# Optimization experiments

Hardware: AMD Instinct MI355X
Metric: run time of the kernel (lower is better)

The kernel has to match this reference:

```python
import jax, jax.numpy as jnp
import numpy as np

B, P, M = 16, 16384, 2048
D_Z, D_PHI, D_R = 512, 256, 64
H1, H2 = 96, 96
IN_DIM = D_Z + 3 * D_PHI + D_R  # 1344


def setup_inputs() -> dict:
    key = jax.random.key(0)
    ks = jax.random.split(key, 8)
    g_q = jax.random.normal(ks[0], (B, D_Z), dtype=jnp.float32)
    Phi = jax.random.normal(ks[1], (M, D_PHI), dtype=jnp.float32)
    # pair indices with i < j (sort each row)
    pi = jax.random.randint(ks[2], (P, 2), 0, M, dtype=jnp.int64)
    pair_index = jnp.sort(pi, axis=-1)
    relation_features = jax.random.normal(ks[3], (P, D_R), dtype=jnp.float32)
    # learned MLP params (Linear weights stored [in, out])
    W1 = jax.random.normal(ks[4], (IN_DIM, H1), dtype=jnp.float32) / np.sqrt(IN_DIM)
    b1 = jnp.zeros((H1,), dtype=jnp.float32)
    W2 = jax.random.normal(ks[5], (H1, H2), dtype=jnp.float32) / np.sqrt(H1)
    b2 = jnp.zeros((H2,), dtype=jnp.float32)
    W3 = jax.random.normal(ks[6], (H2, 1), dtype=jnp.float32) / np.sqrt(H2)
    b3 = jnp.zeros((1,), dtype=jnp.float32)
    return {"g_q": g_q, "Phi": Phi, "pair_index": pair_index,
            "relation_features": relation_features,
            "W1": W1, "b1": b1, "W2": W2, "b2": b2, "W3": W3, "b3": b3}


def reference(g_q, Phi, pair_index, relation_features, W1, b1, W2, b2, W3, b3):
    # gather pair embeddings: [P, d_phi]
    phi_i = Phi[pair_index[:, 0]]
    phi_j = Phi[pair_index[:, 1]]
    # symmetric combine -> [P, 3*d_phi + d_r]
    pair_feats = jnp.concatenate(
        [phi_i + phi_j, jnp.abs(phi_i - phi_j), phi_i * phi_j, relation_features],
        axis=-1)
    b, p = g_q.shape[0], pair_feats.shape[0]
    # broadcast-concat -> x: [B, P, in_dim]
    x = jnp.concatenate(
        [jnp.broadcast_to(g_q[:, None, :], (b, p, g_q.shape[-1])),
         jnp.broadcast_to(pair_feats[None, :, :], (b, p, pair_feats.shape[-1]))],
        axis=-1)
    # small MLP: Linear -> GELU (erf, dropout is identity at eval) x2, then Linear(->1)
    h = jax.nn.gelu(x @ W1 + b1, approximate=False)
    h = jax.nn.gelu(h @ W2 + b2, approximate=False)
    out = h @ W3 + b3  # [B, P, 1]
    return out[..., 0]  # [B, P]
```

## Files before the change

kernel.cpp:

```cpp
#include <hip/hip_runtime.h>
#include <hip/hip_bf16.h>
#include <stdint.h>

static constexpr int P_N   = 16384;
static constexpr int D_Z   = 512;
static constexpr int D_PHI = 256;
static constexpr int D_R   = 64;
static constexpr int H     = 96;
static constexpr int KP    = 832;

using f32x4 = __attribute__((ext_vector_type(4))) float;
using s16x8 = __attribute__((ext_vector_type(8))) short;

__device__ __forceinline__ unsigned short f2bf(float f) {
    union { float f; uint32_t u; } v; v.f = f;
    return (unsigned short)((v.u + 0x7FFFu + ((v.u >> 16) & 1u)) >> 16);
}

__device__ __forceinline__ uint32_t pkbf2(float lo, float hi) {
    union { __hip_bfloat162 h; uint32_t u; } c;
    c.h = __float22bfloat162_rn(make_float2(lo, hi));
    return c.u;
}

__device__ __forceinline__ float gelu_f(float x) {
    float x2 = x * x;
    float u  = __builtin_fmaf(-0.1029444f, x2, -2.3022126f);
    float e  = __builtin_amdgcn_exp2f(x * u);
    return x * __builtin_amdgcn_rcpf(1.0f + e);
}

__global__ __launch_bounds__(256) void prep_kernel(
    const float* __restrict__ g_q, const float* __restrict__ W1,
    const float* __restrict__ b1, const float* __restrict__ W2,
    float* __restrict__ gqfrag, unsigned short* __restrict__ W1frag,
    unsigned short* __restrict__ W2frag)
{
    __shared__ float gql[D_Z];
    __shared__ float red[192];
    const int blk = blockIdx.x;
    const int t = threadIdx.x;
    if (blk < 16) {
        const int b = blk;
        for (int i = t; i < D_Z; i += 256) gql[i] = g_q[b * D_Z + i];
        __syncthreads();
        float acc = 0.f;
        if (t < 192) {
            const int n = t % 96, s = t / 96;
            const int k0 = s * 256;
            #pragma unroll 8
            for (int k = 0; k < 256; ++k)
                acc += gql[k0 + k] * W1[(k0 + k) * H + n];
            red[t] = acc;
        }
        __syncthreads();
        if (t < 96) {
            const float v = red[t] + red[t + 96] + b1[t];
            const int dst = ((t >> 5) * 64 + ((t >> 3) & 3) * 16 + b) * 8 + (t & 7);
            gqfrag[dst] = v;
        }
    } else if (blk < 328) {
        const int e = (blk - 16) * 256 + t;
        const int n = e / KP, k = e % KP;
        const int nf = n >> 4, lr = n & 15;
        const int kc = k >> 5, l4 = (k >> 3) & 3, ke = k & 7;
        W1frag[((nf * 26 + kc) * 64 + l4 * 16 + lr) * 8 + ke] =
            f2bf(W1[(D_Z + k) * H + n]);
    } else {
        const int e = (blk - 328) * 256 + t;
        const int n = e / H, k = e % H;
        const int nf = n >> 4, lr = n & 15;
        const int ks = k >> 5, l4 = (k >> 3) & 3, ke = k & 7;
        W2frag[((nf * 3 + ks) * 64 + l4 * 16 + lr) * 8 + ke] =
            f2bf(W2[k * H + n]);
    }
}

__global__ __launch_bounds__(512, 2) void fused11_kernel(
    const float* __restrict__ Phi, const int* __restrict__ pidx,
    const float* __restrict__ rel, const unsigned short* __restrict__ W1frag,
    const float* __restrict__ gqfrag, const unsigned short* __restrict__ W2frag,
    const float* __restrict__ b2, const float* __restrict__ W3,
    const float* __restrict__ b3, float* __restrict__ out)
{
    constexpr int FS = 840;
    __shared__ __align__(16) unsigned short feats[16 * FS];
    __shared__ __align__(16) float y1part[2][16][100];
    const int t = threadIdx.x;
    const int p0 = blockIdx.x * 16;

    {
        const int p = t >> 5, c = t & 31, kb = c * 8;
        const int2 ij = *(const int2*)(pidx + 2 * (p0 + p));
        const float* PI = Phi + (long)ij.x * D_PHI + kb;
        const float* PJ = Phi + (long)ij.y * D_PHI + kb;
        float4 a0 = *(const float4*)PI, a1 = *(const float4*)(PI + 4);
        float4 c0 = *(const float4*)PJ, c1 = *(const float4*)(PJ + 4);
        uint4 s, d, q;
        s.x = pkbf2(a0.x + c0.x, a0.y + c0.y);
        s.y = pkbf2(a0.z + c0.z, a0.w + c0.w);
        s.z = pkbf2(a1.x + c1.x, a1.y + c1.y);
        s.w = pkbf2(a1.z + c1.z, a1.w + c1.w);
        d.x = pkbf2(fabsf(a0.x - c0.x), fabsf(a0.y - c0.y));
        d.y = pkbf2(fabsf(a0.z - c0.z), fabsf(a0.w - c0.w));
        d.z = pkbf2(fabsf(a1.x - c1.x), fabsf(a1.y - c1.y));
        d.w = pkbf2(fabsf(a1.z - c1.z), fabsf(a1.w - c1.w));
        q.x = pkbf2(a0.x * c0.x, a0.y * c0.y);
        q.y = pkbf2(a0.z * c0.z, a0.w * c0.w);
        q.z = pkbf2(a1.x * c1.x, a1.y * c1.y);
        q.w = pkbf2(a1.z * c1.z, a1.w * c1.w);
        *(uint4*)&feats[p * FS + kb]       = s;
        *(uint4*)&feats[p * FS + 256 + kb] = d;
        *(uint4*)&feats[p * FS + 512 + kb] = q;
        if (t < 128) {
            const int p2 = t >> 3, c2 = t & 7;
            const float* R = rel + (long)(p0 + p2) * D_R + c2 * 8;
            float4 r0 = *(const float4*)R, r1 = *(const float4*)(R + 4);
            uint4 rr;
            rr.x = pkbf2(r0.x, r0.y); rr.y = pkbf2(r0.z, r0.w);
            rr.z = pkbf2(r1.x, r1.y); rr.w = pkbf2(r1.z, r1.w);
            *(uint4*)&feats[p2 * FS + 768 + c2 * 8] = rr;
        }
    }
    __syncthreads();

    const int w  = t >> 6;
    const int l  = t & 63;
    const int lr = l & 15, l4 = l >> 4;

    if (w < 6) {
        const int kh = w & 1, ng = w >> 1;
        const int kc0 = kh * 13;
        f32x4 acc[2];
        acc[0] = (f32x4){0.f,0.f,0.f,0.f};
        acc[1] = (f32x4){0.f,0.f,0.f,0.f};
        const unsigned short* Arow = &feats[lr * FS + l4 * 8];
        for (int kc = kc0; kc < kc0 + 13; ++kc) {
            const s16x8 a = *(const s16x8*)(Arow + kc * 32);
            #pragma unroll
            for (int j = 0; j < 2; ++j) {
                const s16x8 bb = *(const s16x8*)(W1frag +
                    (((ng * 2 + j) * 26 + kc) * 64 + l) * 8);
                acc[j] = __builtin_amdgcn_mfma_f32_16x16x32_bf16(a, bb, acc[j], 0, 0, 0);
            }
        }
        #pragma unroll
        for (int j = 0; j < 2; ++j)
            #pragma unroll
            for (int r = 0; r < 4; ++r)
                y1part[kh][l4 * 4 + r][ng * 32 + j * 16 + lr] = acc[j][r];
    }
    __syncthreads();

    float part[2][4];
    #pragma unroll
    for (int mf = 0; mf < 2; ++mf) {
        const int pl = 2 * w + mf;

        s16x8 afr[3];
        #pragma unroll
        for (int ks = 0; ks < 3; ++ks) {
            const int c = ks * 32 + l4 * 8;
            const float* gp = gqfrag + (ks * 64 + l) * 8;
            float4 g0 = *(const float4*)gp, g1 = *(const float4*)(gp + 4);
            const float* ya = &y1part[0][pl][c];
            const float* yb = &y1part[1][pl][c];
            float4 u0 = *(const float4*)ya, u1 = *(const float4*)(ya + 4);
            float4 v0 = *(const float4*)yb, v1 = *(const float4*)(yb + 4);
            union { s16x8 v; uint32_t u[4]; } pk;
            pk.u[0] = pkbf2(gelu_f(g0.x + u0.x + v0.x), gelu_f(g0.y + u0.y + v0.y));
            pk.u[1] = pkbf2(gelu_f(g0.z + u0.z + v0.z), gelu_f(g0.w + u0.w + v0.w));
            pk.u[2] = pkbf2(gelu_f(g1.x + u1.x + v1.x), gelu_f(g1.y + u1.y + v1.y));
            pk.u[3] = pkbf2(gelu_f(g1.z + u1.z + v1.z), gelu_f(g1.w + u1.w + v1.w));
            afr[ks] = pk.v;
        }

        f32x4 acc2[6];
        #pragma unroll
        for (int nf = 0; nf < 6; ++nf) {
            const float bv = b2[nf * 16 + lr];
            acc2[nf] = (f32x4){bv, bv, bv, bv};
        }
        #pragma unroll
        for (int ks = 0; ks < 3; ++ks) {
            #pragma unroll
            for (int nf = 0; nf < 6; ++nf) {
                const s16x8 bb = *(const s16x8*)(W2frag + ((nf * 3 + ks) * 64 + l) * 8);
                acc2[nf] = __builtin_amdgcn_mfma_f32_16x16x32_bf16(afr[ks], bb, acc2[nf], 0, 0, 0);
            }
        }

        part[mf][0] = part[mf][1] = part[mf][2] = part[mf][3] = 0.f;
        #pragma unroll
        for (int nf = 0; nf < 6; ++nf) {
            const float wv = W3[nf * 16 + lr];
            #pragma unroll
            for (int r4 = 0; r4 < 4; ++r4)
                part[mf][r4] = __builtin_fmaf(gelu_f(acc2[nf][r4]), wv, part[mf][r4]);
        }
    }

    #pragma unroll
    for (int mask = 1; mask <= 8; mask <<= 1)
        #pragma unroll
        for (int mf = 0; mf < 2; ++mf)
            #pragma unroll
            for (int r4 = 0; r4 < 4; ++r4)
                part[mf][r4] += __shfl_xor(part[mf][r4], mask, 64);
    if (lr == 0) {
        const float b3v = b3[0];
        #pragma unroll
        for (int mf = 0; mf < 2; ++mf)
            #pragma unroll
            for (int r4 = 0; r4 < 4; ++r4)
                out[(l4 * 4 + r4) * P_N + p0 + 2 * w + mf] = part[mf][r4] + b3v;
    }
}

extern "C" void kernel_launch(void* const* d_in, const int* in_sizes, int n_in,
                              void* d_out, int out_size, void* d_ws, size_t ws_size,
                              hipStream_t stream)
{
    const float* g_q  = (const float*)d_in[0];
    const float* Phi  = (const float*)d_in[1];
    const int*   pidx = (const int*)d_in[2];
    const float* rel  = (const float*)d_in[3];
    const float* W1   = (const float*)d_in[4];
    const float* b1   = (const float*)d_in[5];
    const float* W2   = (const float*)d_in[6];
    const float* b2   = (const float*)d_in[7];
    const float* W3   = (const float*)d_in[8];
    const float* b3   = (const float*)d_in[9];
    float* out = (float*)d_out;

    char* ws = (char*)d_ws;
    float*          gqfrag = (float*)(ws + 0);
    unsigned short* W1frag = (unsigned short*)(ws + 8192);
    unsigned short* W2frag = (unsigned short*)(ws + 167936);

    hipLaunchKernelGGL(prep_kernel, dim3(364), dim3(256), 0, stream,
                       g_q, W1, b1, W2, gqfrag, W1frag, W2frag);
    hipLaunchKernelGGL(fused11_kernel, dim3(P_N / 16), dim3(512), 0, stream,
                       Phi, pidx, rel, W1frag, gqfrag, W2frag, b2, W3, b3, out);
}
```

Baseline: 42.92 us.

## Process two pair tiles per block with register prefetch of next tile's gathers

Each block now handles two 16-pair tiles instead of one, halving the grid. While the current tile's MFMA layers run, the Phi/relation gathers for the next tile are issued into registers and written to shared memory after the tile finishes. The aim is to hide gather latency behind compute. The cost is extra live registers, an additional barrier per tile, and only 512 blocks, which may underfill the GPU's CUs.

```diff
diff --git a/kernel.cpp b/kernel.cpp
--- a/kernel.cpp
+++ b/kernel.cpp
@@ -76,144 +76,164 @@
     }
 }
 
-__global__ __launch_bounds__(512, 2) void fused11_kernel(
+__global__ __launch_bounds__(512, 2) void fused14_kernel(
     const float* __restrict__ Phi, const int* __restrict__ pidx,
     const float* __restrict__ rel, const unsigned short* __restrict__ W1frag,
     const float* __restrict__ gqfrag, const unsigned short* __restrict__ W2frag,
     const float* __restrict__ b2, const float* __restrict__ W3,
     const float* __restrict__ b3, float* __restrict__ out)
 {
-    constexpr int FS = 840;
+    constexpr int FS  = 840;
+    constexpr int TPB = 2;
     __shared__ __align__(16) unsigned short feats[16 * FS];
     __shared__ __align__(16) float y1part[2][16][100];
     const int t = threadIdx.x;
-    const int p0 = blockIdx.x * 16;
-
-    {
-        const int p = t >> 5, c = t & 31, kb = c * 8;
-        const int2 ij = *(const int2*)(pidx + 2 * (p0 + p));
-        const float* PI = Phi + (long)ij.x * D_PHI + kb;
-        const float* PJ = Phi + (long)ij.y * D_PHI + kb;
-        float4 a0 = *(const float4*)PI, a1 = *(const float4*)(PI + 4);
-        float4 c0 = *(const float4*)PJ, c1 = *(const float4*)(PJ + 4);
+    const int tile0 = blockIdx.x * TPB;
+
+    const int w  = t >> 6;
+    const int l  = t & 63;
+    const int lr = l & 15, l4 = l >> 4;
+
+    const int sp = t >> 5, sc = t & 31, skb = sc * 8;
+    const int rp = t >> 3, rc = t & 7;
+    float4 a0, a1, c0v, c1v, r0, r1;
+
+    auto LOAD = [&](int tile) {
+        const int p0 = tile * 16;
+        const int2 ij = *(const int2*)(pidx + 2 * (p0 + sp));
+        const float* PI = Phi + (long)ij.x * D_PHI + skb;
+        const float* PJ = Phi + (long)ij.y * D_PHI + skb;
+        a0  = *(const float4*)PI;  a1  = *(const float4*)(PI + 4);
+        c0v = *(const float4*)PJ;  c1v = *(const float4*)(PJ + 4);
+        if (t < 128) {
+            const float* R = rel + (long)(p0 + rp) * D_R + rc * 8;
+            r0 = *(const float4*)R; r1 = *(const float4*)(R + 4);
+        }
+    };
+    auto STORE_FEATS = [&]() {
         uint4 s, d, q;
-        s.x = pkbf2(a0.x + c0.x, a0.y + c0.y);
-        s.y = pkbf2(a0.z + c0.z, a0.w + c0.w);
-        s.z = pkbf2(a1.x + c1.x, a1.y + c1.y);
-        s.w = pkbf2(a1.z + c1.z, a1.w + c1.w);
-        d.x = pkbf2(fabsf(a0.x - c0.x), fabsf(a0.y - c0.y));
-        d.y = pkbf2(fabsf(a0.z - c0.z), fabsf(a0.w - c0.w));
-        d.z = pkbf2(fabsf(a1.x - c1.x), fabsf(a1.y - c1.y));
-        d.w = pkbf2(fabsf(a1.z - c1.z), fabsf(a1.w - c1.w));
-        q.x = pkbf2(a0.x * c0.x, a0.y * c0.y);
-        q.y = pkbf2(a0.z * c0.z, a0.w * c0.w);
-        q.z = pkbf2(a1.x * c1.x, a1.y * c1.y);
-        q.w = pkbf2(a1.z * c1.z, a1.w * c1.w);
-        *(uint4*)&feats[p * FS + kb]       = s;
-        *(uint4*)&feats[p * FS + 256 + kb] = d;
-        *(uint4*)&feats[p * FS + 512 + kb] = q;
+        s.x = pkbf2(a0.x + c0v.x, a0.y + c0v.y);
+        s.y = pkbf2(a0.z + c0v.z, a0.w + c0v.w);
+        s.z = pkbf2(a1.x + c1v.x, a1.y + c1v.y);
+        s.w = pkbf2(a1.z + c1v.z, a1.w + c1v.w);
+        d.x = pkbf2(fabsf(a0.x - c0v.x), fabsf(a0.y - c0v.y));
+        d.y = pkbf2(fabsf(a0.z - c0v.z), fabsf(a0.w - c0v.w));
+        d.z = pkbf2(fabsf(a1.x - c1v.x), fabsf(a1.y - c1v.y));
+        d.w = pkbf2(fabsf(a1.z - c1v.z), fabsf(a1.w - c1v.w));
+        q.x = pkbf2(a0.x * c0v.x, a0.y * c0v.y);
+        q.y = pkbf2(a0.z * c0v.z, a0.w * c0v.w);
+        q.z = pkbf2(a1.x * c1v.x, a1.y * c1v.y);
+        q.w = pkbf2(a1.z * c1v.z, a1.w * c1v.w);
+        *(uint4*)&feats[sp * FS + skb]       = s;
+        *(uint4*)&feats[sp * FS + 256 + skb] = d;
+        *(uint4*)&feats[sp * FS + 512 + skb] = q;
         if (t < 128) {
-            const int p2 = t >> 3, c2 = t & 7;
-            const float* R = rel + (long)(p0 + p2) * D_R + c2 * 8;
-            float4 r0 = *(const float4*)R, r1 = *(const float4*)(R + 4);
             uint4 rr;
             rr.x = pkbf2(r0.x, r0.y); rr.y = pkbf2(r0.z, r0.w);
             rr.z = pkbf2(r1.x, r1.y); rr.w = pkbf2(r1.z, r1.w);
-            *(uint4*)&feats[p2 * FS + 768 + c2 * 8] = rr;
-        }
-    }
+            *(uint4*)&feats[rp * FS + 768 + rc * 8] = rr;
+        }
+    };
+
+    LOAD(tile0);
+    STORE_FEATS();
     __syncthreads();
 
-    const int w  = t >> 6;
-    const int l  = t & 63;
-    const int lr = l & 15, l4 = l >> 4;
-
-    if (w < 6) {
-        const int kh = w & 1, ng = w >> 1;
-        const int kc0 = kh * 13;
-        f32x4 acc[2];
-        acc[0] = (f32x4){0.f,0.f,0.f,0.f};
-        acc[1] = (f32x4){0.f,0.f,0.f,0.f};
-        const unsigned short* Arow = &feats[lr * FS + l4 * 8];
-        for (int kc = kc0; kc < kc0 + 13; ++kc) {
-            const s16x8 a = *(const s16x8*)(Arow + kc * 32);
-            #pragma unroll
-            for (int j = 0; j < 2; ++j) {
-                const s16x8 bb = *(const s16x8*)(W1frag +
-                    (((ng * 2 + j) * 26 + kc) * 64 + l) * 8);
-                acc[j] = __builtin_amdgcn_mfma_f32_16x16x32_bf16(a, bb, acc[j], 0, 0, 0);
-            }
-        }
+    for (int tt = 0; tt < TPB; ++tt) {
+        const int p0 = (tile0 + tt) * 16;
+
+        if (tt + 1 < TPB) LOAD(tile0 + tt + 1);
+
+        if (w < 6) {
+            const int kh = w & 1, ng = w >> 1;
+            const int kc0 = kh * 13;
+            f32x4 acc[2];
+            acc[0] = (f32x4){0.f,0.f,0.f,0.f};
+            acc[1] = (f32x4){0.f,0.f,0.f,0.f};
+            const unsigned short* Arow = &feats[lr * FS + l4 * 8];
+            for (int kc = kc0; kc < kc0 + 13; ++kc) {
+                const s16x8 a = *(const s16x8*)(Arow + kc * 32);
+                #pragma unroll
+                for (int j = 0; j < 2; ++j) {
+                    const s16x8 bb = *(const s16x8*)(W1frag +
+                        (((ng * 2 + j) * 26 + kc) * 64 + l) * 8);
+                    acc[j] = __builtin_amdgcn_mfma_f32_16x16x32_bf16(a, bb, acc[j], 0, 0, 0);
+                }
+            }
+            #pragma unroll
+            for (int j = 0; j < 2; ++j)
+                #pragma unroll
+                for (int r = 0; r < 4; ++r)
+                    y1part[kh][l4 * 4 + r][ng * 32 + j * 16 + lr] = acc[j][r];
+        }
+        __syncthreads();
+
+        float part[2][4];
         #pragma unroll
-        for (int j = 0; j < 2; ++j)
-            #pragma unroll
-            for (int r = 0; r < 4; ++r)
-                y1part[kh][l4 * 4 + r][ng * 32 + j * 16 + lr] = acc[j][r];
-    }
-    __syncthreads();
-
-    float part[2][4];
-    #pragma unroll
-    for (int mf = 0; mf < 2; ++mf) {
-        const int pl = 2 * w + mf;
-
-        s16x8 afr[3];
+        for (int mf = 0; mf < 2; ++mf) {
+            const int pl = 2 * w + mf;
+
+            s16x8 afr[3];
+            #pragma unroll
+            for (int ks = 0; ks < 3; ++ks) {
+                const int c = ks * 32 + l4 * 8;
+                const float* gp = gqfrag + (ks * 64 + l) * 8;
+                float4 g0 = *(const float4*)gp, g1 = *(const float4*)(gp + 4);
+                const float* ya = &y1part[0][pl][c];
+                const float* yb = &y1part[1][pl][c];
+                float4 u0 = *(const float4*)ya, u1 = *(const float4*)(ya + 4);
+                float4 v0 = *(const float4*)yb, v1 = *(const float4*)(yb + 4);
+                union { s16x8 v; uint32_t u[4]; } pk;
+                pk.u[0] = pkbf2(gelu_f(g0.x + u0.x + v0.x), gelu_f(g0.y + u0.y + v0.y));
+                pk.u[1] = pkbf2(gelu_f(g0.z + u0.z + v0.z), gelu_f(g0.w + u0.w + v0.w));
+                pk.u[2] = pkbf2(gelu_f(g1.x + u1.x + v1.x), gelu_f(g1.y + u1.y + v1.y));
+                pk.u[3] = pkbf2(gelu_f(g1.z + u1.z + v1.z), gelu_f(g1.w + u1.w + v1.w));
+                afr[ks] = pk.v;
+            }
+
+            f32x4 acc2[6];
+            #pragma unroll
+            for (int nf = 0; nf < 6; ++nf) {
+                const float bv = b2[nf * 16 + lr];
+                acc2[nf] = (f32x4){bv, bv, bv, bv};
+            }
+            #pragma unroll
+            for (int ks = 0; ks < 3; ++ks) {
+                #pragma unroll
+                for (int nf = 0; nf < 6; ++nf) {
+                    const s16x8 bb = *(const s16x8*)(W2frag + ((nf * 3 + ks) * 64 + l) * 8);
+                    acc2[nf] = __builtin_amdgcn_mfma_f32_16x16x32_bf16(afr[ks], bb, acc2[nf], 0, 0, 0);
+                }
+            }
+
+            part[mf][0] = part[mf][1] = part[mf][2] = part[mf][3] = 0.f;
+            #pragma unroll
+            for (int nf = 0; nf < 6; ++nf) {
+                const float wv = W3[nf * 16 + lr];
+                #pragma unroll
+                for (int r4 = 0; r4 < 4; ++r4)
+                    part[mf][r4] = __builtin_fmaf(gelu_f(acc2[nf][r4]), wv, part[mf][r4]);
+            }
+        }
+
         #pragma unroll
-        for (int ks = 0; ks < 3; ++ks) {
-            const int c = ks * 32 + l4 * 8;
-            const float* gp = gqfrag + (ks * 64 + l) * 8;
-            float4 g0 = *(const float4*)gp, g1 = *(const float4*)(gp + 4);
-            const float* ya = &y1part[0][pl][c];
-            const float* yb = &y1part[1][pl][c];
-            float4 u0 = *(const float4*)ya, u1 = *(const float4*)(ya + 4);
-            float4 v0 = *(const float4*)yb, v1 = *(const float4*)(yb + 4);
-            union { s16x8 v; uint32_t u[4]; } pk;
-            pk.u[0] = pkbf2(gelu_f(g0.x + u0.x + v0.x), gelu_f(g0.y + u0.y + v0.y));
-            pk.u[1] = pkbf2(gelu_f(g0.z + u0.z + v0.z), gelu_f(g0.w + u0.w + v0.w));
-            pk.u[2] = pkbf2(gelu_f(g1.x + u1.x + v1.x), gelu_f(g1.y + u1.y + v1.y));
-            pk.u[3] = pkbf2(gelu_f(g1.z + u1.z + v1.z), gelu_f(g1.w + u1.w + v1.w));
-            afr[ks] = pk.v;
-        }
-
-        f32x4 acc2[6];
-        #pragma unroll
-        for (int nf = 0; nf < 6; ++nf) {
-            const float bv = b2[nf * 16 + lr];
-            acc2[nf] = (f32x4){bv, bv, bv, bv};
-        }
-        #pragma unroll
-        for (int ks = 0; ks < 3; ++ks) {
-            #pragma unroll
-            for (int nf = 0; nf < 6; ++nf) {
-                const s16x8 bb = *(const s16x8*)(W2frag + ((nf * 3 + ks) * 64 + l) * 8);
-                acc2[nf] = __builtin_amdgcn_mfma_f32_16x16x32_bf16(afr[ks], bb, acc2[nf], 0, 0, 0);
-            }
-        }
-
-        part[mf][0] = part[mf][1] = part[mf][2] = part[mf][3] = 0.f;
-        #pragma unroll
-        for (int nf = 0; nf < 6; ++nf) {
-            const float wv = W3[nf * 16 + lr];
-            #pragma unroll
-            for (int r4 = 0; r4 < 4; ++r4)
-                part[mf][r4] = __builtin_fmaf(gelu_f(acc2[nf][r4]), wv, part[mf][r4]);
-        }
-    }
-
-    #pragma unroll
-    for (int mask = 1; mask <= 8; mask <<= 1)
-        #pragma unroll
-        for (int mf = 0; mf < 2; ++mf)
-            #pragma unroll
-            for (int r4 = 0; r4 < 4; ++r4)
-                part[mf][r4] += __shfl_xor(part[mf][r4], mask, 64);
-    if (lr == 0) {
-        const float b3v = b3[0];
-        #pragma unroll
-        for (int mf = 0; mf < 2; ++mf)
-            #pragma unroll
-            for (int r4 = 0; r4 < 4; ++r4)
-                out[(l4 * 4 + r4) * P_N + p0 + 2 * w + mf] = part[mf][r4] + b3v;
+        for (int mask = 1; mask <= 8; mask <<= 1)
+            #pragma unroll
+            for (int mf = 0; mf < 2; ++mf)
+                #pragma unroll
+                for (int r4 = 0; r4 < 4; ++r4)
+                    part[mf][r4] += __shfl_xor(part[mf][r4], mask, 64);
+        if (lr == 0) {
+            const float b3v = b3[0];
+            #pragma unroll
+            for (int mf = 0; mf < 2; ++mf)
+                #pragma unroll
+                for (int r4 = 0; r4 < 4; ++r4)
+                    out[(l4 * 4 + r4) * P_N + p0 + 2 * w + mf] = part[mf][r4] + b3v;
+        }
+
+        if (tt + 1 < TPB) STORE_FEATS();
+        __syncthreads();
     }
 }
 
@@ -240,6 +260,6 @@
 
     hipLaunchKernelGGL(prep_kernel, dim3(364), dim3(256), 0, stream,
                        g_q, W1, b1, W2, gqfrag, W1frag, W2frag);
-    hipLaunchKernelGGL(fused11_kernel, dim3(P_N / 16), dim3(512), 0, stream,
+    hipLaunchKernelGGL(fused14_kernel, dim3(P_N / 32), dim3(512), 0, stream,
                        Phi, pidx, rel, W1frag, gqfrag, W2frag, b2, W3, b3, out);
 }
```

Result: slower. 137.3 us (+219.8%).

## Process 32 pairs per block so each W1 fragment load feeds two MFMAs

Applied to the files above, without the earlier changes.

Each block now handles 32 pairs instead of 16. The gather phase loops twice, and the layer-1 MFMA loop accumulates two 16-row tiles so every W1frag load from global is reused for both. Layer 2 and 3 loop over four pairs per wave and reduce and store after each. The aim is to halve W1 weight traffic and per-block overhead, at the cost of roughly double the LDS use (about 79KB), which may limit occupancy to a single block per CU, and half as many blocks.

```diff
diff --git a/kernel.cpp b/kernel.cpp
--- a/kernel.cpp
+++ b/kernel.cpp
@@ -76,7 +76,7 @@
     }
 }
 
-__global__ __launch_bounds__(512, 2) void fused11_kernel(
+__global__ __launch_bounds__(512, 2) void fused15_kernel(
     const float* __restrict__ Phi, const int* __restrict__ pidx,
     const float* __restrict__ rel, const unsigned short* __restrict__ W1frag,
     const float* __restrict__ gqfrag, const unsigned short* __restrict__ W2frag,
@@ -84,13 +84,15 @@
     const float* __restrict__ b3, float* __restrict__ out)
 {
     constexpr int FS = 840;
-    __shared__ __align__(16) unsigned short feats[16 * FS];
-    __shared__ __align__(16) float y1part[2][16][100];
+    __shared__ __align__(16) unsigned short feats[32 * FS];
+    __shared__ __align__(16) float y1part[2][32][100];
     const int t = threadIdx.x;
-    const int p0 = blockIdx.x * 16;
-
-    {
-        const int p = t >> 5, c = t & 31, kb = c * 8;
+    const int p0 = blockIdx.x * 32;
+
+    #pragma unroll
+    for (int it = 0; it < 2; ++it) {
+        const int task = t + it * 512;
+        const int p = task >> 5, c = task & 31, kb = c * 8;
         const int2 ij = *(const int2*)(pidx + 2 * (p0 + p));
         const float* PI = Phi + (long)ij.x * D_PHI + kb;
         const float* PJ = Phi + (long)ij.y * D_PHI + kb;
@@ -112,15 +114,15 @@
         *(uint4*)&feats[p * FS + kb]       = s;
         *(uint4*)&feats[p * FS + 256 + kb] = d;
         *(uint4*)&feats[p * FS + 512 + kb] = q;
-        if (t < 128) {
-            const int p2 = t >> 3, c2 = t & 7;
-            const float* R = rel + (long)(p0 + p2) * D_R + c2 * 8;
-            float4 r0 = *(const float4*)R, r1 = *(const float4*)(R + 4);
-            uint4 rr;
-            rr.x = pkbf2(r0.x, r0.y); rr.y = pkbf2(r0.z, r0.w);
-            rr.z = pkbf2(r1.x, r1.y); rr.w = pkbf2(r1.z, r1.w);
-            *(uint4*)&feats[p2 * FS + 768 + c2 * 8] = rr;
-        }
+    }
+    if (t < 256) {
+        const int p2 = t >> 3, c2 = t & 7;
+        const float* R = rel + (long)(p0 + p2) * D_R + c2 * 8;
+        float4 r0 = *(const float4*)R, r1 = *(const float4*)(R + 4);
+        uint4 rr;
+        rr.x = pkbf2(r0.x, r0.y); rr.y = pkbf2(r0.z, r0.w);
+        rr.z = pkbf2(r1.x, r1.y); rr.w = pkbf2(r1.z, r1.w);
+        *(uint4*)&feats[p2 * FS + 768 + c2 * 8] = rr;
     }
     __syncthreads();
 
@@ -131,31 +133,39 @@
     if (w < 6) {
         const int kh = w & 1, ng = w >> 1;
         const int kc0 = kh * 13;
-        f32x4 acc[2];
-        acc[0] = (f32x4){0.f,0.f,0.f,0.f};
-        acc[1] = (f32x4){0.f,0.f,0.f,0.f};
-        const unsigned short* Arow = &feats[lr * FS + l4 * 8];
+        f32x4 acc[2][2];
+        #pragma unroll
+        for (int m = 0; m < 2; ++m)
+            #pragma unroll
+            for (int j = 0; j < 2; ++j)
+                acc[m][j] = (f32x4){0.f,0.f,0.f,0.f};
+        const unsigned short* A0 = &feats[lr * FS + l4 * 8];
+        const unsigned short* A1 = &feats[(16 + lr) * FS + l4 * 8];
         for (int kc = kc0; kc < kc0 + 13; ++kc) {
-            const s16x8 a = *(const s16x8*)(Arow + kc * 32);
+            const s16x8 a0 = *(const s16x8*)(A0 + kc * 32);
+            const s16x8 a1 = *(const s16x8*)(A1 + kc * 32);
             #pragma unroll
             for (int j = 0; j < 2; ++j) {
                 const s16x8 bb = *(const s16x8*)(W1frag +
                     (((ng * 2 + j) * 26 + kc) * 64 + l) * 8);
-                acc[j] = __builtin_amdgcn_mfma_f32_16x16x32_bf16(a, bb, acc[j], 0, 0, 0);
+                acc[0][j] = __builtin_amdgcn_mfma_f32_16x16x32_bf16(a0, bb, acc[0][j], 0, 0, 0);
+                acc[1][j] = __builtin_amdgcn_mfma_f32_16x16x32_bf16(a1, bb, acc[1][j], 0, 0, 0);
             }
         }
         #pragma unroll
-        for (int j = 0; j < 2; ++j)
-            #pragma unroll
-            for (int r = 0; r < 4; ++r)
-                y1part[kh][l4 * 4 + r][ng * 32 + j * 16 + lr] = acc[j][r];
+        for (int m = 0; m < 2; ++m)
+            #pragma unroll
+            for (int j = 0; j < 2; ++j)
+                #pragma unroll
+                for (int r = 0; r < 4; ++r)
+                    y1part[kh][m * 16 + l4 * 4 + r][ng * 32 + j * 16 + lr] = acc[m][j][r];
     }
     __syncthreads();
 
-    float part[2][4];
+    const float b3v = b3[0];
     #pragma unroll
-    for (int mf = 0; mf < 2; ++mf) {
-        const int pl = 2 * w + mf;
+    for (int mf = 0; mf < 4; ++mf) {
+        const int pl = 4 * w + mf;
 
         s16x8 afr[3];
         #pragma unroll
@@ -190,30 +200,24 @@
             }
         }
 
-        part[mf][0] = part[mf][1] = part[mf][2] = part[mf][3] = 0.f;
+        float part[4] = {0.f, 0.f, 0.f, 0.f};
         #pragma unroll
         for (int nf = 0; nf < 6; ++nf) {
             const float wv = W3[nf * 16 + lr];
             #pragma unroll
             for (int r4 = 0; r4 < 4; ++r4)
-                part[mf][r4] = __builtin_fmaf(gelu_f(acc2[nf][r4]), wv, part[mf][r4]);
-        }
-    }
-
-    #pragma unroll
-    for (int mask = 1; mask <= 8; mask <<= 1)
-        #pragma unroll
-        for (int mf = 0; mf < 2; ++mf)
+                part[r4] = __builtin_fmaf(gelu_f(acc2[nf][r4]), wv, part[r4]);
+        }
+        #pragma unroll
+        for (int mask = 1; mask <= 8; mask <<= 1)
             #pragma unroll
             for (int r4 = 0; r4 < 4; ++r4)
-                part[mf][r4] += __shfl_xor(part[mf][r4], mask, 64);
-    if (lr == 0) {
-        const float b3v = b3[0];
-        #pragma unroll
-        for (int mf = 0; mf < 2; ++mf)
+                part[r4] += __shfl_xor(part[r4], mask, 64);
+        if (lr == 0) {
             #pragma unroll
             for (int r4 = 0; r4 < 4; ++r4)
-                out[(l4 * 4 + r4) * P_N + p0 + 2 * w + mf] = part[mf][r4] + b3v;
+                out[(l4 * 4 + r4) * P_N + p0 + pl] = part[r4] + b3v;
+        }
     }
 }
 
@@ -240,6 +244,6 @@
 
     hipLaunchKernelGGL(prep_kernel, dim3(364), dim3(256), 0, stream,
                        g_q, W1, b1, W2, gqfrag, W1frag, W2frag);
-    hipLaunchKernelGGL(fused11_kernel, dim3(P_N / 16), dim3(512), 0, stream,
+    hipLaunchKernelGGL(fused15_kernel, dim3(P_N / 32), dim3(512), 0, stream,
                        Phi, pidx, rel, W1frag, gqfrag, W2frag, b2, W3, b3, out);
 }
```

Measured after the change: 37.96 us, median of 2. 1.13x faster.
